# Kernel tuning notes

Measured on AMD Instinct MI355X. Metric: run time of the kernel, lower is better.

Reference implementation:

```python
import jax, jax.numpy as jnp
import numpy as np

B, S, D, E = 8, 2048, 1024, 8
TOKENS = B * S
CAPACITY = TOKENS // E  # capacity_factor=1.0, top-1 gating (deepspeed default)


def _moe_layer(x_flat, Wg, We, be):
    """DeepSpeed-style top-1 MoE: gate -> capacity drop -> dispatch -> expert GEMM -> combine.
    x_flat: [T, D]; Wg: [D, E]; We: [E, D, D]; be: [E, D]."""
    gates = jax.nn.softmax(x_flat @ Wg, axis=-1)              # [T, E]
    idx = jnp.argmax(gates, axis=1)                            # [T] expert per token
    mask = jax.nn.one_hot(idx, E, dtype=jnp.int32)             # [T, E]
    loc = jnp.cumsum(mask, axis=0) - 1                         # position within expert
    loc_s = jnp.sum(loc * mask, axis=1)                        # [T]
    keep = loc_s < CAPACITY                                    # capacity drop
    gate_s = jnp.sum(gates * mask.astype(gates.dtype), axis=1) * keep.astype(gates.dtype)
    slot = jnp.clip(loc_s, 0, CAPACITY - 1)
    # dispatch: scatter kept tokens into [E, C, D] buffer (slots are unique for kept tokens)
    disp = jnp.zeros((E, CAPACITY, D), x_flat.dtype).at[idx, slot].add(
        x_flat * keep[:, None].astype(x_flat.dtype))
    # grouped expert GEMM
    eo = jnp.einsum('ecd,edf->ecf', disp, We) + be[:, None, :]  # [E, C, D]
    # combine: gather each token's expert output, scale by its gate value
    return eo[idx, slot] * gate_s[:, None]                      # [T, D]


def reference(x, y, W1, b1, Wg2, We2, be2, Wg3, We3, be3):
    h = jnp.einsum('bsd,df->bsf', x, W1) + b1                  # dense pre-layer
    hf = h.reshape(TOKENS, D)
    o = _moe_layer(hf, Wg2, We2, be2)
    o = _moe_layer(o, Wg3, We3, be3)
    h = h + o.reshape(B, S, D)                                 # residual add
    sent = h.mean(axis=1)                                      # [B, D]
    logp = jax.nn.log_softmax(sent, axis=-1)
    return -jnp.mean(logp[jnp.arange(B), y])                   # CrossEntropyLoss


def setup_inputs() -> dict:
    key = jax.random.key(0)
    ks = jax.random.split(key, 10)
    s = 0.02
    return {
        'x': jax.random.normal(ks[0], (B, S, D), jnp.float32),
        'y': jax.random.randint(ks[1], (B,), 0, D),
        'W1': jax.random.normal(ks[2], (D, D), jnp.float32) * s,
        'b1': jnp.zeros((D,), jnp.float32),
        'Wg2': jax.random.normal(ks[3], (D, E), jnp.float32) * s,
        'We2': jax.random.normal(ks[4], (E, D, D), jnp.float32) * s,
        'be2': jnp.zeros((E, D), jnp.float32),
        'Wg3': jax.random.normal(ks[5], (D, E), jnp.float32) * s,
        'We3': jax.random.normal(ks[6], (E, D, D), jnp.float32) * s,
        'be3': jnp.zeros((E, D), jnp.float32),
    }
```

## Files before the change

kernel.cpp:

```cpp
#include <hip/hip_runtime.h>
#include <hip/hip_bf16.h>
#include <math.h>


#define TOKS 16384
#define DIM 1024
#define NEXP 8
#define CAP 2048
#define BATCH 8
#define SEQ 2048

typedef __bf16 bf16_t;
typedef __bf16 bf16x8 __attribute__((ext_vector_type(8)));
typedef float fx4 __attribute__((ext_vector_type(4)));

__device__ __forceinline__ void gll16(const bf16_t* g, bf16_t* l) {
  __builtin_amdgcn_global_load_lds(
      (const __attribute__((address_space(1))) unsigned int*)g,
      (__attribute__((address_space(3))) unsigned int*)l, 16, 0, 0);
}

#define BARRIER() asm volatile("s_barrier" ::: "memory")
#define LGKM0()   asm volatile("s_waitcnt lgkmcnt(0)" ::: "memory")
#define VMC(N)    asm volatile("s_waitcnt vmcnt(" #N ")" ::: "memory")

#define PW_BLOCKS (17 * 256)
#define CVT_BLOCKS (TOKS * DIM / 8 / 256)
#define PREP_GRID (PW_BLOCKS + 2 + CVT_BLOCKS + 1)
__global__ __launch_bounds__(256) void k_prep(
    const float* __restrict__ W1, const float* __restrict__ We2,
    const float* __restrict__ We3, const float* __restrict__ Wg2,
    const float* __restrict__ Wg3, const float* __restrict__ x,
    bf16_t* __restrict__ Wt, bf16_t* __restrict__ WgP,
    bf16_t* __restrict__ xb, uint4* __restrict__ zreg, int znq) {
  const int id = blockIdx.x;
  const int tid = threadIdx.x;
  if (id < PW_BLOCKS) {
    __shared__ float t[64][65];
    const int m = id >> 8, rem = id & 255;
    const int n0 = (rem & 15) * 64, k0 = (rem >> 4) * 64;
    const float* src = (m == 0) ? W1
                       : (m <= 8) ? We2 + (size_t)(m - 1) * DIM * DIM
                                  : We3 + (size_t)(m - 9) * DIM * DIM;
    bf16_t* dst = Wt + (size_t)m * DIM * DIM;
    const int r = tid >> 4, c4 = (tid & 15) * 4;
#pragma unroll
    for (int i = 0; i < 4; i++) {
      float4 v = *(const float4*)&src[(size_t)(k0 + i * 16 + r) * DIM + n0 + c4];
      t[i * 16 + r][c4] = v.x;
      t[i * 16 + r][c4 + 1] = v.y;
      t[i * 16 + r][c4 + 2] = v.z;
      t[i * 16 + r][c4 + 3] = v.w;
    }
    __syncthreads();
#pragma unroll
    for (int i = 0; i < 4; i++) {
      int rn = i * 16 + r;
      union { bf16_t b[4]; uint2 u; } tmp;
#pragma unroll
      for (int j = 0; j < 4; j++) tmp.b[j] = (bf16_t)t[c4 + j][rn];
      *(uint2*)&dst[(size_t)(n0 + rn) * DIM + k0 + c4] = tmp.u;
    }
  } else if (id < PW_BLOCKS + 2) {
    const int which = id - PW_BLOCKS;
    const float* src = which ? Wg3 : Wg2;
    bf16_t* dst = WgP + which * (128 * 8 * 8);
#pragma unroll
    for (int j = 0; j < 4; j++) {
      int d = tid * 4 + j;
      float4 a = *(const float4*)&src[d * 8];
      float4 b = *(const float4*)&src[d * 8 + 4];
      float v[8] = {a.x, a.y, a.z, a.w, b.x, b.y, b.z, b.w};
#pragma unroll
      for (int e = 0; e < 8; e++)
        dst[((d >> 3) * 8 + e) * 8 + (d & 7)] = (bf16_t)v[e];
    }
  } else if (id < PW_BLOCKS + 2 + CVT_BLOCKS) {
    const int cid = id - PW_BLOCKS - 2;
    size_t i = ((size_t)cid * 256 + tid) * 8;
    float4 a = *(const float4*)&x[i];
    float4 b = *(const float4*)&x[i + 4];
    union { bf16_t h[8]; uint4 u; } t;
    t.h[0] = (bf16_t)a.x; t.h[1] = (bf16_t)a.y; t.h[2] = (bf16_t)a.z; t.h[3] = (bf16_t)a.w;
    t.h[4] = (bf16_t)b.x; t.h[5] = (bf16_t)b.y; t.h[6] = (bf16_t)b.z; t.h[7] = (bf16_t)b.w;
    *(uint4*)&xb[i] = t.u;
  } else {
    const uint4 z = {0u, 0u, 0u, 0u};
    for (int i = tid; i < znq; i += 256) zreg[i] = z;
  }
}

template <int MODE>
__global__ __launch_bounds__(512) void k_gemm256(
    const bf16_t* __restrict__ A, const bf16_t* __restrict__ Bt0,
    const float* __restrict__ bias0, bf16_t* __restrict__ out,
    float* __restrict__ sent, const int* __restrict__ tok,
    const int* __restrict__ cnt, const float* __restrict__ gate,
    const bf16_t* __restrict__ zp) {
  __shared__ alignas(16) bf16_t As[2][256 * 64];
  __shared__ alignas(16) bf16_t Bs[2][256 * 64];
  const int tid = threadIdx.x;
  const int lane = tid & 63, wave = tid >> 6;
  const int quad = lane >> 4, l15 = lane & 15;
  const int wm = wave >> 2, wn = wave & 3;
  const int id = blockIdx.x;
  const int xcd = id & 7, rem = id >> 3;
  const int n0 = (rem & 3) * 256;

  int m0;
  int count = 0;
  const bf16_t* Bt;
  const float* bias;
  const int* tk = nullptr;
  if constexpr (MODE == 0) {
    m0 = (xcd * 8 + (rem >> 2)) * 256;
    Bt = Bt0;
    bias = bias0;
  } else {
    m0 = (rem >> 2) * 256;
    count = cnt[xcd];
    if (m0 >= count) return;
    Bt = Bt0 + (size_t)xcd * DIM * DIM;
    bias = bias0 + xcd * DIM;
    tk = tok + xcd * CAP;
  }

  const int kc = (tid & 7) ^ ((tid >> 3) & 7);
  const int rbase = tid >> 3;

  const bf16_t* gA[4];
  const bf16_t* gB[4];
#pragma unroll
  for (int h = 0; h < 2; h++)
#pragma unroll
    for (int i = 0; i < 2; i++) {
      const int r = h * 128 + i * 64 + rbase;
      if constexpr (MODE == 0) {
        gA[h * 2 + i] = A + (size_t)(m0 + r) * DIM + kc * 8;
      } else {
        const int ca = m0 + r;
        gA[h * 2 + i] = (ca < count) ? A + (size_t)tk[ca] * DIM + kc * 8 : zp;
      }
      gB[h * 2 + i] = Bt + (size_t)(n0 + r) * DIM + kc * 8;
    }

  auto stA = [&](int t, int half) {
#pragma unroll
    for (int i = 0; i < 2; i++)
      gll16(gA[half * 2 + i] + t * 64,
            &As[t & 1][(half * 128 + i * 64 + wave * 8) * 64]);
  };
  auto stB = [&](int t, int half) {
#pragma unroll
    for (int i = 0; i < 2; i++)
      gll16(gB[half * 2 + i] + t * 64,
            &Bs[t & 1][(half * 128 + i * 64 + wave * 8) * 64]);
  };
  auto rdA = [&](bf16x8 (&av)[4][2], int buf, int mh) {
#pragma unroll
    for (int mf = 0; mf < 4; mf++)
#pragma unroll
      for (int s = 0; s < 2; s++)
        av[mf][s] = *(const bf16x8*)&As[buf][(wm * 128 + (mh * 4 + mf) * 16 + l15) * 64 +
                                            (((s * 4 + quad) ^ (l15 & 7)) << 3)];
  };
  auto rdB = [&](bf16x8 (&bv)[2][2], int buf, int nh) {
#pragma unroll
    for (int nf = 0; nf < 2; nf++)
#pragma unroll
      for (int s = 0; s < 2; s++)
        bv[nf][s] = *(const bf16x8*)&Bs[buf][(wn * 64 + (nh * 2 + nf) * 16 + l15) * 64 +
                                            (((s * 4 + quad) ^ (l15 & 7)) << 3)];
  };

  fx4 acc[8][4];
#pragma unroll
  for (int i = 0; i < 8; i++)
#pragma unroll
    for (int j = 0; j < 4; j++) acc[i][j] = (fx4)0.0f;

  auto mma = [&](bf16x8 (&av)[4][2], bf16x8 (&bv)[2][2], int mh, int nh) {
    __builtin_amdgcn_s_setprio(1);
#pragma unroll
    for (int s = 0; s < 2; s++)
#pragma unroll
      for (int mf = 0; mf < 4; mf++)
#pragma unroll
        for (int nf = 0; nf < 2; nf++)
          acc[mh * 4 + mf][nh * 2 + nf] = __builtin_amdgcn_mfma_f32_16x16x32_bf16(
              av[mf][s], bv[nf][s], acc[mh * 4 + mf][nh * 2 + nf], 0, 0, 0);
    __builtin_amdgcn_s_setprio(0);
  };

  stA(0, 0); stA(0, 1); stB(0, 0); stB(0, 1);
  stB(1, 0); stB(1, 1); stA(1, 0);
  VMC(6);
  BARRIER();

  bf16x8 av0[4][2], av1[4][2], bv0[2][2], bv1[2][2];
#pragma unroll 2
  for (int t = 0; t < 14; t++) {
    const int buf = t & 1;
    rdA(av0, buf, 0); rdB(bv0, buf, 0); rdB(bv1, buf, 1);
    stA(t + 1, 1);
    BARRIER(); LGKM0();
    mma(av0, bv0, 0, 0);
    BARRIER();
    stB(t + 2, 0);
    BARRIER();
    mma(av0, bv1, 0, 1);
    BARRIER();
    rdA(av1, buf, 1);
    stB(t + 2, 1);
    BARRIER(); LGKM0();
    mma(av1, bv1, 1, 1);
    BARRIER();
    stA(t + 2, 0);
    mma(av1, bv0, 1, 0);
    VMC(6);
    BARRIER();
  }
  {
    rdA(av0, 0, 0); rdB(bv0, 0, 0); rdB(bv1, 0, 1);
    stA(15, 1);
    BARRIER(); LGKM0();
    mma(av0, bv0, 0, 0);
    BARRIER();
    mma(av0, bv1, 0, 1);
    BARRIER();
    rdA(av1, 0, 1);
    BARRIER(); LGKM0();
    mma(av1, bv1, 1, 1);
    BARRIER();
    mma(av1, bv0, 1, 0);
    VMC(0);
    BARRIER();
  }
  {
    rdA(av0, 1, 0); rdB(bv0, 1, 0); rdB(bv1, 1, 1); rdA(av1, 1, 1);
    LGKM0();
    mma(av0, bv0, 0, 0); mma(av0, bv1, 0, 1);
    mma(av1, bv1, 1, 1); mma(av1, bv0, 1, 0);
  }

  float bb[4];
#pragma unroll
  for (int nf = 0; nf < 4; nf++) bb[nf] = bias[n0 + wn * 64 + nf * 16 + l15];
  if constexpr (MODE == 0) {
    float sj[4] = {0.f, 0.f, 0.f, 0.f};
#pragma unroll
    for (int mf = 0; mf < 8; mf++)
#pragma unroll
      for (int r = 0; r < 4; r++) {
        const int rowL = wm * 128 + mf * 16 + quad * 4 + r;
#pragma unroll
        for (int nf = 0; nf < 4; nf++) {
          const float v = acc[mf][nf][r] + bb[nf];
          sj[nf] += v;
          out[(size_t)(m0 + rowL) * DIM + n0 + wn * 64 + nf * 16 + l15] = (bf16_t)v;
        }
      }
#pragma unroll
    for (int nf = 0; nf < 4; nf++) {
      sj[nf] += __shfl_xor(sj[nf], 16);
      sj[nf] += __shfl_xor(sj[nf], 32);
    }
    if (quad == 0)
#pragma unroll
      for (int nf = 0; nf < 4; nf++)
        atomicAdd(&sent[(m0 >> 11) * DIM + n0 + wn * 64 + nf * 16 + l15],
                  sj[nf] * (1.0f / SEQ));
  } else {
#pragma unroll
    for (int mf = 0; mf < 8; mf++)
#pragma unroll
      for (int r = 0; r < 4; r++) {
        const int c = m0 + wm * 128 + mf * 16 + quad * 4 + r;
        if (c < count) {
          const int tkn = tk[c];
          const float g = gate[tkn];
#pragma unroll
          for (int nf = 0; nf < 4; nf++)
            out[(size_t)tkn * DIM + n0 + wn * 64 + nf * 16 + l15] =
                (bf16_t)((acc[mf][nf][r] + bb[nf]) * g);
        }
      }
  }
}

__global__ __launch_bounds__(256) void k_gate_mm(
    const bf16_t* __restrict__ act, const bf16_t* __restrict__ WgPx,
    int* __restrict__ idx, float* __restrict__ gate) {
  __shared__ alignas(16) bf16_t As[64 * 64];
  __shared__ alignas(16) bf16_t WgS[128 * 64];
  __shared__ float L[64][8];
  const int tid = threadIdx.x;
  const int lane = tid & 63, wave = tid >> 6;
  const int quad = lane >> 4, l15 = lane & 15;
  const int m0 = blockIdx.x * 64;
  const int kc = (tid & 7) ^ ((tid >> 3) & 7);
  const int rbase = tid >> 3;

#pragma unroll
  for (int j = 0; j < 4; j++)
    gll16(WgPx + (j * 256 + wave * 64 + lane) * 8, &WgS[(j * 256 + wave * 64) * 8]);

  const bf16_t* gA[2]; bf16_t* lA[2];
#pragma unroll
  for (int i = 0; i < 2; i++) {
    gA[i] = act + (size_t)(m0 + rbase + 32 * i) * DIM + kc * 8;
    lA[i] = &As[wave * 512 + i * 2048];
  }
  fx4 acc = (fx4)0.0f;
  for (int k0 = 0; k0 < DIM; k0 += 64) {
#pragma unroll
    for (int i = 0; i < 2; i++) gll16(gA[i] + k0, lA[i]);
    __syncthreads();
#pragma unroll
    for (int s = 0; s < 2; s++) {
      const int pofs = ((s * 4 + quad) ^ (l15 & 7)) << 3;
      bf16x8 av = *(const bf16x8*)&As[(wave * 16 + l15) * 64 + pofs];
      bf16x8 bv = *(const bf16x8*)&WgS[((k0 >> 3) + s * 4 + quad) * 64 + (l15 & 7) * 8];
      acc = __builtin_amdgcn_mfma_f32_16x16x32_bf16(av, bv, acc, 0, 0, 0);
    }
    __syncthreads();
  }
  if (l15 < 8) {
#pragma unroll
    for (int r = 0; r < 4; r++) L[wave * 16 + quad * 4 + r][l15] = acc[r];
  }
  __syncthreads();
  if (tid < 64) {
    float lg[8];
#pragma unroll
    for (int e = 0; e < 8; e++) lg[e] = L[tid][e];
    float best = lg[0];
    int bi = 0;
#pragma unroll
    for (int e = 1; e < 8; e++)
      if (lg[e] > best) { best = lg[e]; bi = e; }
    float s = 0.f;
#pragma unroll
    for (int e = 0; e < 8; e++) s += expf(lg[e] - best);
    idx[m0 + tid] = bi;
    gate[m0 + tid] = 1.0f / s;
  }
}

#define DLMAX 2048
__global__ __launch_bounds__(1024) void k_route(
    const int* __restrict__ idx, int* __restrict__ tok, int* __restrict__ cnt,
    bf16_t* __restrict__ obuf) {
  const int e = blockIdx.x;
  const int tid = threadIdx.x, lane = tid & 63, wv = tid >> 6;
  __shared__ int wsum[16];
  __shared__ int dlist[DLMAX];
  const int4* p = (const int4*)(idx + tid * 16);
  int m[16];
  int c = 0;
#pragma unroll
  for (int j = 0; j < 4; j++) {
    int4 v = p[j];
    m[j * 4 + 0] = (v.x == e);
    m[j * 4 + 1] = (v.y == e);
    m[j * 4 + 2] = (v.z == e);
    m[j * 4 + 3] = (v.w == e);
    c += m[j * 4] + m[j * 4 + 1] + m[j * 4 + 2] + m[j * 4 + 3];
  }
  int sc = c;
#pragma unroll
  for (int off = 1; off < 64; off <<= 1) {
    int n = __shfl_up(sc, off);
    if (lane >= off) sc += n;
  }
  if (lane == 63) wsum[wv] = sc;
  __syncthreads();
  int wb = 0, tot = 0;
#pragma unroll
  for (int i = 0; i < 16; i++) {
    int s = wsum[i];
    tot += s;
    if (i < wv) wb += s;
  }
  int pos = wb + sc - c;
  const uint4 z = {0u, 0u, 0u, 0u};
#pragma unroll
  for (int j = 0; j < 16; j++) {
    if (m[j]) {
      int t = tid * 16 + j;
      if (pos < CAP) {
        tok[e * CAP + pos] = t;
      } else {
        int di = pos - CAP;
        if (di < DLMAX) dlist[di] = t;
        else
          for (int k = 0; k < 128; k++) *(uint4*)&obuf[(size_t)t * DIM + k * 8] = z;
      }
      pos++;
    }
  }
  if (tid == 0) cnt[e] = tot < CAP ? tot : CAP;
  __syncthreads();
  int ndl = tot - CAP;
  ndl = ndl < 0 ? 0 : (ndl > DLMAX ? DLMAX : ndl);
  for (int d = tid >> 7; d < ndl; d += 8) {
    int t = dlist[d];
    *(uint4*)&obuf[(size_t)t * DIM + (tid & 127) * 8] = z;
  }
}

__global__ __launch_bounds__(256) void k_reduce_loss(
    const bf16_t* __restrict__ o2, const float* __restrict__ sent,
    float* __restrict__ sentP, const int* __restrict__ y,
    int* __restrict__ done, float* __restrict__ out) {
  const int tid = threadIdx.x;
  {
    const int job = blockIdx.x;
    const int d8 = (tid & 127) * 8;
    const int sg = tid >> 7;
    const int b = job >> 5;
    const int s0 = (job & 31) * 64 + sg * 32;
    float acc[8] = {0.f, 0.f, 0.f, 0.f, 0.f, 0.f, 0.f, 0.f};
    const size_t base = ((size_t)b * SEQ + s0) * DIM + d8;
#pragma unroll 1
    for (int i0 = 0; i0 < 32; i0 += 8) {
      uint4 u[8];
#pragma unroll
      for (int i = 0; i < 8; i++)
        u[i] = *(const uint4*)&o2[base + (size_t)(i0 + i) * DIM];
#pragma unroll
      for (int i = 0; i < 8; i++) {
        union { bf16_t v[8]; uint4 q; } oo;
        oo.q = u[i];
#pragma unroll
        for (int j = 0; j < 8; j++) acc[j] += (float)oo.v[j];
      }
    }
    float* dst = sentP + (size_t)(job * 2 + sg) * DIM + d8;
    float4 lo = {acc[0], acc[1], acc[2], acc[3]};
    float4 hi = {acc[4], acc[5], acc[6], acc[7]};
    *(float4*)dst = lo;
    *(float4*)(dst + 4) = hi;
  }
  __shared__ int isLast;
  __syncthreads();
  if (tid == 0) {
    __threadfence();
    isLast = (atomicAdd(done, 1) == (int)gridDim.x - 1);
  }
  __syncthreads();
  if (!isLast) return;
  __threadfence();
  __shared__ float finL[DIM];
  __shared__ float red[256];
  float total = 0.f;
  for (int b = 0; b < BATCH; b++) {
    const int c4 = tid * 4;
    float4 t4 = {0.f, 0.f, 0.f, 0.f};
    const float* pb = sentP + (size_t)b * 64 * DIM + c4;
#pragma unroll 1
    for (int r0 = 0; r0 < 64; r0 += 8) {
      float4 u[8];
#pragma unroll
      for (int r = 0; r < 8; r++) u[r] = *(const float4*)&pb[(size_t)(r0 + r) * DIM];
#pragma unroll
      for (int r = 0; r < 8; r++) {
        t4.x += u[r].x; t4.y += u[r].y; t4.z += u[r].z; t4.w += u[r].w;
      }
    }
    float4 s4 = *(const float4*)&sent[b * DIM + c4];
    float f0 = s4.x + t4.x * (1.0f / SEQ);
    float f1 = s4.y + t4.y * (1.0f / SEQ);
    float f2 = s4.z + t4.z * (1.0f / SEQ);
    float f3 = s4.w + t4.w * (1.0f / SEQ);
    finL[c4] = f0; finL[c4 + 1] = f1; finL[c4 + 2] = f2; finL[c4 + 3] = f3;
    float m = fmaxf(fmaxf(f0, f1), fmaxf(f2, f3));
    red[tid] = m;
    __syncthreads();
    for (int s = 128; s; s >>= 1) {
      if (tid < s) red[tid] = fmaxf(red[tid], red[tid + s]);
      __syncthreads();
    }
    m = red[0];
    __syncthreads();
    float sum = expf(f0 - m) + expf(f1 - m) + expf(f2 - m) + expf(f3 - m);
    red[tid] = sum;
    __syncthreads();
    for (int s = 128; s; s >>= 1) {
      if (tid < s) red[tid] += red[tid + s];
      __syncthreads();
    }
    if (tid == 0) total += m + logf(red[0]) - finL[y[b]];
    __syncthreads();
  }
  if (tid == 0) out[0] = total * (1.0f / BATCH);
}

extern "C" void kernel_launch(void* const* d_in, const int* in_sizes, int n_in,
                              void* d_out, int out_size, void* d_ws, size_t ws_size,
                              hipStream_t stream) {
  (void)in_sizes; (void)n_in; (void)out_size; (void)ws_size;
  const float* x   = (const float*)d_in[0];
  const int*   y   = (const int*)d_in[1];
  const float* W1  = (const float*)d_in[2];
  const float* b1  = (const float*)d_in[3];
  const float* Wg2 = (const float*)d_in[4];
  const float* We2 = (const float*)d_in[5];
  const float* be2 = (const float*)d_in[6];
  const float* Wg3 = (const float*)d_in[7];
  const float* We3 = (const float*)d_in[8];
  const float* be3 = (const float*)d_in[9];

  char* p = (char*)d_ws;
  size_t off = 0;
  auto carve = [&](size_t bytes) -> char* {
    char* r = p + off;
    off += (bytes + 255) & ~(size_t)255;
    return r;
  };
  bf16_t* Wt   = (bf16_t*)carve((size_t)17 * DIM * DIM * 2);
  bf16_t* WgP  = (bf16_t*)carve(2 * 128 * 8 * 8 * 2);
  bf16_t* h    = (bf16_t*)carve((size_t)TOKS * DIM * 2);
  bf16_t* o1   = (bf16_t*)carve((size_t)TOKS * DIM * 2);
  bf16_t* o2   = (bf16_t*)carve((size_t)TOKS * DIM * 2);
  int*    idx  = (int*)carve(TOKS * 4);
  float*  gate = (float*)carve(TOKS * 4);
  int*    tok  = (int*)carve(NEXP * CAP * 4);
  int*    cnt  = (int*)carve(NEXP * 4);
  size_t zoff0 = off;
  float*  sent = (float*)carve(BATCH * DIM * 4);
  bf16_t* zp   = (bf16_t*)carve(4096);
  int*    done = (int*)carve(256);
  size_t zbytes = off - zoff0;
  float*  sentP = (float*)carve((size_t)512 * DIM * 4);
  bf16_t* xb   = o2;

  k_prep<<<PREP_GRID, 256, 0, stream>>>(
      W1, We2, We3, Wg2, Wg3, x, Wt, WgP, xb,
      (uint4*)sent, (int)(zbytes / 16));

  k_gemm256<0><<<256, 512, 0, stream>>>(
      xb, Wt, b1, h, sent, nullptr, nullptr, nullptr, zp);

  k_gate_mm<<<TOKS / 64, 256, 0, stream>>>(h, WgP, idx, gate);
  k_route<<<NEXP, 1024, 0, stream>>>(idx, tok, cnt, o1);
  k_gemm256<1><<<256, 512, 0, stream>>>(
      h, Wt + (size_t)1 * DIM * DIM, be2, o1, nullptr, tok, cnt, gate, zp);

  k_gate_mm<<<TOKS / 64, 256, 0, stream>>>(o1, WgP + 128 * 8 * 8, idx, gate);
  k_route<<<NEXP, 1024, 0, stream>>>(idx, tok, cnt, o2);
  k_gemm256<1><<<256, 512, 0, stream>>>(
      o1, Wt + (size_t)9 * DIM * DIM, be3, o2, nullptr, tok, cnt, gate, zp);

  k_reduce_loss<<<256, 256, 0, stream>>>(o2, sent, sentP, y, done, (float*)d_out);
}
```

Measured before the change: 398.8 us.

## Split final reduction into per-batch hierarchical last-block reductions

The loss-reduction kernel now runs 512 blocks, each summing 32 rows. The two half-block partials are combined in LDS before one row is written per block. A per-batch counter lets the last block of each batch finish that batch's mean in parallel, and a second counter lets one block compute the log-softmax loss from the per-batch results. This is meant to shorten the serial tail in which a single block reduced all 512 partial rows, at the cost of more atomics and an extra global buffer.

Measured after the change: 369.1 us. 1.08x faster.

```diff
diff --git a/kernel.cpp b/kernel.cpp
--- a/kernel.cpp
+++ b/kernel.cpp
@@ -411,19 +411,21 @@
 
 __global__ __launch_bounds__(256) void k_reduce_loss(
     const bf16_t* __restrict__ o2, const float* __restrict__ sent,
-    float* __restrict__ sentP, const int* __restrict__ y,
-    int* __restrict__ done, float* __restrict__ out) {
+    float* __restrict__ sentP, float* __restrict__ sentF,
+    const int* __restrict__ y, int* __restrict__ done,
+    float* __restrict__ out) {
   const int tid = threadIdx.x;
+  const int job = blockIdx.x;
+  const int b = job >> 6;
+  __shared__ float lds[2][DIM];
   {
-    const int job = blockIdx.x;
     const int d8 = (tid & 127) * 8;
     const int sg = tid >> 7;
-    const int b = job >> 5;
-    const int s0 = (job & 31) * 64 + sg * 32;
+    const int s0 = (job & 63) * 32 + sg * 16;
     float acc[8] = {0.f, 0.f, 0.f, 0.f, 0.f, 0.f, 0.f, 0.f};
     const size_t base = ((size_t)b * SEQ + s0) * DIM + d8;
 #pragma unroll 1
-    for (int i0 = 0; i0 < 32; i0 += 8) {
+    for (int i0 = 0; i0 < 16; i0 += 8) {
       uint4 u[8];
 #pragma unroll
       for (int i = 0; i < 8; i++)
@@ -436,28 +438,32 @@
         for (int j = 0; j < 8; j++) acc[j] += (float)oo.v[j];
       }
     }
-    float* dst = sentP + (size_t)(job * 2 + sg) * DIM + d8;
-    float4 lo = {acc[0], acc[1], acc[2], acc[3]};
-    float4 hi = {acc[4], acc[5], acc[6], acc[7]};
-    *(float4*)dst = lo;
-    *(float4*)(dst + 4) = hi;
-  }
-  __shared__ int isLast;
+#pragma unroll
+    for (int j = 0; j < 8; j++) lds[sg][d8 + j] = acc[j];
+  }
+  __syncthreads();
+  {
+    const int c4 = tid * 4;
+    float4 s;
+    s.x = lds[0][c4] + lds[1][c4];
+    s.y = lds[0][c4 + 1] + lds[1][c4 + 1];
+    s.z = lds[0][c4 + 2] + lds[1][c4 + 2];
+    s.w = lds[0][c4 + 3] + lds[1][c4 + 3];
+    *(float4*)&sentP[(size_t)job * DIM + c4] = s;
+  }
+  __shared__ int isLastB;
   __syncthreads();
   if (tid == 0) {
     __threadfence();
-    isLast = (atomicAdd(done, 1) == (int)gridDim.x - 1);
-  }
-  __syncthreads();
-  if (!isLast) return;
+    isLastB = (atomicAdd(&done[b], 1) == 63);
+  }
+  __syncthreads();
+  if (!isLastB) return;
   __threadfence();
-  __shared__ float finL[DIM];
-  __shared__ float red[256];
-  float total = 0.f;
-  for (int b = 0; b < BATCH; b++) {
+  {
     const int c4 = tid * 4;
     float4 t4 = {0.f, 0.f, 0.f, 0.f};
-    const float* pb = sentP + (size_t)b * 64 * DIM + c4;
+    const float* pb = sentP + (size_t)(b * 64) * DIM + c4;
 #pragma unroll 1
     for (int r0 = 0; r0 < 64; r0 += 8) {
       float4 u[8];
@@ -469,12 +475,28 @@
       }
     }
     float4 s4 = *(const float4*)&sent[b * DIM + c4];
-    float f0 = s4.x + t4.x * (1.0f / SEQ);
-    float f1 = s4.y + t4.y * (1.0f / SEQ);
-    float f2 = s4.z + t4.z * (1.0f / SEQ);
-    float f3 = s4.w + t4.w * (1.0f / SEQ);
-    finL[c4] = f0; finL[c4 + 1] = f1; finL[c4 + 2] = f2; finL[c4 + 3] = f3;
-    float m = fmaxf(fmaxf(f0, f1), fmaxf(f2, f3));
+    float4 f;
+    f.x = s4.x + t4.x * (1.0f / SEQ);
+    f.y = s4.y + t4.y * (1.0f / SEQ);
+    f.z = s4.z + t4.z * (1.0f / SEQ);
+    f.w = s4.w + t4.w * (1.0f / SEQ);
+    *(float4*)&sentF[b * DIM + c4] = f;
+  }
+  __shared__ int isLastF;
+  __syncthreads();
+  if (tid == 0) {
+    __threadfence();
+    isLastF = (atomicAdd(&done[8], 1) == 7);
+  }
+  __syncthreads();
+  if (!isLastF) return;
+  __threadfence();
+  __shared__ float red[256];
+  float total = 0.f;
+  for (int bb = 0; bb < BATCH; bb++) {
+    const int c4 = tid * 4;
+    float4 f = *(const float4*)&sentF[bb * DIM + c4];
+    float m = fmaxf(fmaxf(f.x, f.y), fmaxf(f.z, f.w));
     red[tid] = m;
     __syncthreads();
     for (int s = 128; s; s >>= 1) {
@@ -483,14 +505,14 @@
     }
     m = red[0];
     __syncthreads();
-    float sum = expf(f0 - m) + expf(f1 - m) + expf(f2 - m) + expf(f3 - m);
+    float sum = expf(f.x - m) + expf(f.y - m) + expf(f.z - m) + expf(f.w - m);
     red[tid] = sum;
     __syncthreads();
     for (int s = 128; s; s >>= 1) {
       if (tid < s) red[tid] += red[tid + s];
       __syncthreads();
     }
-    if (tid == 0) total += m + logf(red[0]) - finL[y[b]];
+    if (tid == 0) total += m + logf(red[0]) - sentF[bb * DIM + y[bb]];
     __syncthreads();
   }
   if (tid == 0) out[0] = total * (1.0f / BATCH);
@@ -533,6 +555,7 @@
   int*    done = (int*)carve(256);
   size_t zbytes = off - zoff0;
   float*  sentP = (float*)carve((size_t)512 * DIM * 4);
+  float*  sentF = (float*)carve((size_t)BATCH * DIM * 4);
   bf16_t* xb   = o2;
 
   k_prep<<<PREP_GRID, 256, 0, stream>>>(
@@ -552,5 +575,6 @@
   k_gemm256<1><<<256, 512, 0, stream>>>(
       o1, Wt + (size_t)9 * DIM * DIM, be3, o2, nullptr, tok, cnt, gate, zp);
 
-  k_reduce_loss<<<256, 256, 0, stream>>>(o2, sent, sentP, y, done, (float*)d_out);
-}
+  k_reduce_loss<<<512, 256, 0, stream>>>(o2, sent, sentP, sentF, y, done,
+                                         (float*)d_out);
+}
```
